# Optimization experiments

Hardware: AMD Instinct MI355X
Metric: run time of the kernel (lower is better)

The kernel has to match this reference:

```python
import jax, jax.numpy as jnp
import numpy as np

K = 3          # kernel size
STRIDE = 1
# padding=0, dilation=1, groups=1 (torchvision DeformConv2d defaults for args not passed)


def _offset_conv(x, w_off, b_off):
    # plain VALID conv, NCHW / OIHW
    out = jax.lax.conv_general_dilated(
        x, w_off, window_strides=(STRIDE, STRIDE), padding='VALID',
        dimension_numbers=('NCHW', 'OIHW', 'NCHW'))
    return out + b_off[None, :, None, None]


def _bilinear_sample(xp, ys, xs):
    # xp: [B,H,W,C]; ys/xs: [B,KK,Ho,Wo] fractional sample coords
    B, H, W, _ = xp.shape
    y0f = jnp.floor(ys)
    x0f = jnp.floor(xs)
    wy = ys - y0f
    wx = xs - x0f
    y0 = y0f.astype(jnp.int32)
    x0 = x0f.astype(jnp.int32)
    b = jnp.arange(B)[:, None, None, None]

    def gather(yi, xi):
        valid = (yi >= 0) & (yi < H) & (xi >= 0) & (xi < W)
        yc = jnp.clip(yi, 0, H - 1)
        xc = jnp.clip(xi, 0, W - 1)
        return xp[b, yc, xc] * valid[..., None].astype(xp.dtype)

    v00 = gather(y0, x0)
    v01 = gather(y0, x0 + 1)
    v10 = gather(y0 + 1, x0)
    v11 = gather(y0 + 1, x0 + 1)
    w00 = ((1 - wy) * (1 - wx))[..., None]
    w01 = ((1 - wy) * wx)[..., None]
    w10 = (wy * (1 - wx))[..., None]
    w11 = (wy * wx)[..., None]
    return v00 * w00 + v01 * w01 + v10 * w10 + v11 * w11  # [B,KK,Ho,Wo,C]


def _mdconv_block(x, w_off, b_off, weight, bias):
    B, Cin, H, W = x.shape
    KK = K * K
    off_out = _offset_conv(x, w_off, b_off)            # [B, 3*KK, Ho, Wo]
    Ho, Wo = off_out.shape[2], off_out.shape[3]
    o1 = off_out[:, :KK]
    o2 = off_out[:, KK:2 * KK]
    mask = jax.nn.sigmoid(off_out[:, 2 * KK:])          # [B,KK,Ho,Wo]
    # torchvision offset layout: pairs (y, x) per kernel point, built as cat(o1, o2)
    off = jnp.concatenate([o1, o2], axis=1).reshape(B, KK, 2, Ho, Wo)
    off_y, off_x = off[:, :, 0], off[:, :, 1]

    kh = jnp.arange(KK) // K
    kw = jnp.arange(KK) % K
    base_y = jnp.arange(Ho)[None, :] * STRIDE + kh[:, None]   # [KK,Ho]
    base_x = jnp.arange(Wo)[None, :] * STRIDE + kw[:, None]   # [KK,Wo]
    ys = base_y[None, :, :, None].astype(x.dtype) + off_y     # [B,KK,Ho,Wo]
    xs = base_x[None, :, None, :].astype(x.dtype) + off_x

    xp = jnp.transpose(x, (0, 2, 3, 1))                        # [B,H,W,Cin]
    sampled = _bilinear_sample(xp, ys, xs)                     # [B,KK,Ho,Wo,Cin]
    sampled = sampled * mask[..., None]                        # modulation
    w = weight.reshape(weight.shape[0], weight.shape[1], KK)   # [Cout,Cin,KK]
    out = jnp.einsum('bkhwc,ock->bohw', sampled, w)
    out = out + bias[None, :, None, None]
    return jax.nn.relu(out)  # block's activate_func=relu; norm/pool are None


def setup_inputs() -> dict:
    key = jax.random.key(0)
    k1, k2, k3, k4, k5 = jax.random.split(key, 5)
    B, Cin, Cout, H, W = 4, 64, 64, 128, 128
    x = jax.random.normal(k1, (B, Cin, H, W), dtype=jnp.float32)
    # offset/mask conv params (original zero-inits; use small random to exercise sampling)
    w_off = jax.random.normal(k2, (3 * K * K, Cin, K, K), dtype=jnp.float32) * 0.1 / np.sqrt(Cin * K * K)
    b_off = jax.random.normal(k3, (3 * K * K,), dtype=jnp.float32) * 0.1
    fan_in = Cin * K * K
    weight = jax.random.uniform(k4, (Cout, Cin, K, K), dtype=jnp.float32,
                                minval=-1.0, maxval=1.0) / np.sqrt(fan_in)
    bias = jax.random.uniform(k5, (Cout,), dtype=jnp.float32,
                              minval=-1.0, maxval=1.0) / np.sqrt(fan_in)
    return {'x': x, 'w_off': w_off, 'b_off': b_off, 'weight': weight, 'bias': bias}


def reference(x, w_off, b_off, weight, bias):
    return _mdconv_block(x, w_off, b_off, weight, bias)
```

## Files before the change

### kernel.cpp

```cpp
#include <hip/hip_runtime.h>
#include <hip/hip_bf16.h>
#include <math.h>

namespace {
constexpr int Bn = 4, Cin = 64, Cout = 64, Hh = 128, Ww = 128, Ho = 126, Wo = 126;
constexpr int HW = Hh * Ww;
constexpr int WOB = 63;
constexpr int NBLK = Bn * Ho * 2;
constexpr int ROWU = 68;
constexpr int RSTR = 346;
}

typedef __attribute__((ext_vector_type(8))) short bf16x8;
typedef __attribute__((ext_vector_type(4))) float f32x4;

__device__ __forceinline__ unsigned short f2bf(float f) {
    __hip_bfloat16 h = __float2bfloat16(f);
    return __builtin_bit_cast(unsigned short, h);
}
__device__ __forceinline__ float bf2f(unsigned short u) {
    unsigned int v = (unsigned int)u << 16;
    return __builtin_bit_cast(float, v);
}
__device__ __forceinline__ unsigned int f2bf_pk(float lo, float hi) {
    return (unsigned int)f2bf(lo) | ((unsigned int)f2bf(hi) << 16);
}
__device__ __forceinline__ bf16x8 mk8(unsigned int u0, unsigned int u1,
                                      unsigned int u2, unsigned int u3) {
    union { unsigned int u[4]; bf16x8 v; } x;
    x.u[0] = u0; x.u[1] = u1; x.u[2] = u2; x.u[3] = u3;
    return x.v;
}
__device__ __forceinline__ int swz_block(int orig, int nwg) {
    int q = nwg >> 3, r = nwg & 7;
    int xcd = orig & 7, idx = orig >> 3;
    return (xcd < r ? xcd * (q + 1) : r * (q + 1) + (xcd - r) * q) + idx;
}

__global__ __launch_bounds__(256) void prep_transpose_kernel(
    const float* __restrict__ x, const float* __restrict__ w_off,
    const float* __restrict__ weight, unsigned int* __restrict__ xT16,
    unsigned short* __restrict__ wA_hi, unsigned short* __restrict__ wA_lo,
    unsigned short* __restrict__ wOff_hi, unsigned short* __restrict__ wOff_lo)
{
    int blk = blockIdx.x;
    if (blk < 1024) {
        __shared__ float t[64][65];
        int b    = blk >> 8;
        int hw0  = (blk & 255) * 64;
        int lane = (int)(threadIdx.x & 63);
        int w4   = (int)(threadIdx.x >> 6);

        const float* xb = x + b * (Cin * HW) + hw0;
#pragma unroll
        for (int i = 0; i < 16; ++i) {
            int cin = w4 * 16 + i;
            t[cin][lane] = xb[cin * HW + lane];
        }
        __syncthreads();
        unsigned int* dst = xT16 + ((size_t)b * HW + hw0) * 32;
        int px = (int)(threadIdx.x >> 2);
        int c8 = (int)(threadIdx.x & 3) * 8;
#pragma unroll
        for (int i = 0; i < 8; ++i) {
            int cp = c8 + i;
            dst[px * 32 + cp] = f2bf_pk(t[2 * cp][px], t[2 * cp + 1][px]);
        }
    } else {
        int i = (blk - 1024) * 256 + (int)threadIdx.x;
        if (i < 36864) {
            int j = i % 8;  int t = i / 8;
            int l = t % 64; t /= 64;
            int h = t % 2;  t /= 2;
            int w = t % 4;  int k = t / 4;
            int cout = 16 * w + (l & 15);
            int cin  = 32 * h + 8 * (l >> 4) + j;
            float v = weight[cout * 576 + cin * 9 + k];
            unsigned short hi = f2bf(v);
            wA_hi[i] = hi;
            wA_lo[i] = f2bf(v - bf2f(hi));

            int o = cout;
            float vo = o < 27 ? w_off[o * 576 + cin * 9 + k] : 0.f;
            unsigned short oh = f2bf(vo);
            wOff_hi[i] = oh;
            wOff_lo[i] = f2bf(vo - bf2f(oh));
        }
    }
}

__global__ __launch_bounds__(256, 2) void mdcn_kernel(
    const unsigned int* __restrict__ xT16, const float* __restrict__ b_off,
    const unsigned short* __restrict__ wOff_hi,
    const unsigned short* __restrict__ wOff_lo,
    const unsigned short* __restrict__ wA_hi,
    const unsigned short* __restrict__ wA_lo,
    const float* __restrict__ bias, float* __restrict__ out)
{
    __shared__ unsigned int region[32 * RSTR];
    __shared__ unsigned int lds[2][32 * ROWU];
    __shared__ float Ap[27][64];

    int wg   = swz_block(blockIdx.x, NBLK);
    int wid  = __builtin_amdgcn_readfirstlane((int)(threadIdx.x >> 6));
    int lane = (int)(threadIdx.x & 63);
    int b    = wg / 252;
    int rem  = wg - b * 252;
    int ho   = rem >> 1;
    int c0   = (rem & 1) * WOB;
    int x_lo = c0 - 1;
    int pxs  = min(lane, 62);
    int wo   = c0 + pxs;

    const unsigned int* xTb = xT16 + (size_t)b * HW * 32;

    for (int i = 0; i < 11; ++i) {
        int idx4 = (int)threadIdx.x + 256 * i;
        if (idx4 < 2720) {
            int cp4 = (idx4 & 7) * 4;
            int rc  = idx4 >> 3;
            int row = rc / 68;
            int col = rc - row * 68;
            int y = min(max(ho - 1 + row, 0), Hh - 1);
            int x = min(max(x_lo + col, 0), Ww - 1);
            uint4 q = *reinterpret_cast<const uint4*>(xTb + (y * Ww + x) * 32 + cp4);
            region[(cp4 + 0) * RSTR + rc] = q.x;
            region[(cp4 + 1) * RSTR + rc] = q.y;
            region[(cp4 + 2) * RSTR + rc] = q.z;
            region[(cp4 + 3) * RSTR + rc] = q.w;
        }
    }
    __syncthreads();

    {
        int ct = wid & 1;
        int t0 = (wid >> 1) * 2;
        f32x4 acc0 = {0.f, 0.f, 0.f, 0.f}, acc1 = acc0;
        int g4 = (lane >> 4) * 4;

#pragma unroll
        for (int k = 0; k < 9; ++k) {
            int kh = k / 3, kw = k - 3 * kh;
            int roff = (kh + 1) * 68 + 1 + kw;
            const bf16x8* waH = reinterpret_cast<const bf16x8*>(
                wOff_hi + ((k * 4 + ct) * 2) * 512 + lane * 8);
            const bf16x8* waL = reinterpret_cast<const bf16x8*>(
                wOff_lo + ((k * 4 + ct) * 2) * 512 + lane * 8);
            bf16x8 a0h = waH[0], a1h = waH[64];
            bf16x8 a0l = waL[0], a1l = waL[64];
#pragma unroll
            for (int tt = 0; tt < 2; ++tt) {
                int px = 16 * (t0 + tt) + (lane & 15);
                int ci = roff + px;
                bf16x8 b0 = mk8(region[(g4 + 0) * RSTR + ci], region[(g4 + 1) * RSTR + ci],
                                region[(g4 + 2) * RSTR + ci], region[(g4 + 3) * RSTR + ci]);
                bf16x8 b1 = mk8(region[(16 + g4 + 0) * RSTR + ci], region[(16 + g4 + 1) * RSTR + ci],
                                region[(16 + g4 + 2) * RSTR + ci], region[(16 + g4 + 3) * RSTR + ci]);
                f32x4& a = tt ? acc1 : acc0;
                a = __builtin_amdgcn_mfma_f32_16x16x32_bf16(a0h, b0, a, 0, 0, 0);
                a = __builtin_amdgcn_mfma_f32_16x16x32_bf16(a0l, b0, a, 0, 0, 0);
                a = __builtin_amdgcn_mfma_f32_16x16x32_bf16(a1h, b1, a, 0, 0, 0);
                a = __builtin_amdgcn_mfma_f32_16x16x32_bf16(a1l, b1, a, 0, 0, 0);
            }
        }

#pragma unroll
        for (int tt = 0; tt < 2; ++tt) {
            f32x4 a = tt ? acc1 : acc0;
            int px = 16 * (t0 + tt) + (lane & 15);
#pragma unroll
            for (int rg = 0; rg < 4; ++rg) {
                int o = 16 * ct + 4 * (lane >> 4) + rg;
                if (o < 27) Ap[o][px] = a[rg];
            }
        }
        __syncthreads();
    }

    auto SAMPLE = [&](int k, int buf) {
        float oy = Ap[2 * k][lane];
        float ox = Ap[2 * k + 1][lane];
        float mv = Ap[18 + k][lane] + b_off[18 + k];
        float ys = (float)(ho + k / 3) + oy + b_off[2 * k];
        float xs = (float)(wo + k % 3) + ox + b_off[2 * k + 1];
        float m  = 1.0f / (1.0f + expf(-mv));
        float y0f = floorf(ys), x0f = floorf(xs);
        float wy = ys - y0f, wx = xs - x0f;
        int y0 = (int)y0f, x0 = (int)x0f;
        float vy0 = (y0 >= 0  && y0 < Hh)     ? 1.f : 0.f;
        float vy1 = (y0 >= -1 && y0 < Hh - 1) ? 1.f : 0.f;
        float vx0 = (x0 >= 0  && x0 < Ww)     ? 1.f : 0.f;
        float vx1 = (x0 >= -1 && x0 < Ww - 1) ? 1.f : 0.f;
        float W00 = (1.f - wy) * (1.f - wx) * m * vy0 * vx0;
        float W01 = (1.f - wy) * wx         * m * vy0 * vx1;
        float W10 = wy         * (1.f - wx) * m * vy1 * vx0;
        float W11 = wy         * wx         * m * vy1 * vx1;

        unsigned int cu00[8], cu01[8], cu10[8], cu11[8];
        bool ok = (y0 >= ho - 1) && (y0 <= ho + 2) &&
                  (x0 >= x_lo) && (x0 <= x_lo + 66);
        if (ok) {
            int s00 = (y0 - (ho - 1)) * 68 + (x0 - x_lo);
#pragma unroll
            for (int j = 0; j < 8; ++j) {
                int basej = (wid * 8 + j) * RSTR + s00;
                cu00[j] = region[basej];
                cu01[j] = region[basej + 1];
                cu10[j] = region[basej + 68];
                cu11[j] = region[basej + 69];
            }
        } else {
            int y0c = min(max(y0, 0), Hh - 1), y1c = min(max(y0 + 1, 0), Hh - 1);
            int x0c = min(max(x0, 0), Ww - 1), x1c = min(max(x0 + 1, 0), Ww - 1);
            const unsigned int* bw = xTb + wid * 8;
            uint4 qa, qb;
            qa = *reinterpret_cast<const uint4*>(bw + (y0c * Ww + x0c) * 32);
            qb = *reinterpret_cast<const uint4*>(bw + (y0c * Ww + x0c) * 32 + 4);
            cu00[0]=qa.x; cu00[1]=qa.y; cu00[2]=qa.z; cu00[3]=qa.w;
            cu00[4]=qb.x; cu00[5]=qb.y; cu00[6]=qb.z; cu00[7]=qb.w;
            qa = *reinterpret_cast<const uint4*>(bw + (y0c * Ww + x1c) * 32);
            qb = *reinterpret_cast<const uint4*>(bw + (y0c * Ww + x1c) * 32 + 4);
            cu01[0]=qa.x; cu01[1]=qa.y; cu01[2]=qa.z; cu01[3]=qa.w;
            cu01[4]=qb.x; cu01[5]=qb.y; cu01[6]=qb.z; cu01[7]=qb.w;
            qa = *reinterpret_cast<const uint4*>(bw + (y1c * Ww + x0c) * 32);
            qb = *reinterpret_cast<const uint4*>(bw + (y1c * Ww + x0c) * 32 + 4);
            cu10[0]=qa.x; cu10[1]=qa.y; cu10[2]=qa.z; cu10[3]=qa.w;
            cu10[4]=qb.x; cu10[5]=qb.y; cu10[6]=qb.z; cu10[7]=qb.w;
            qa = *reinterpret_cast<const uint4*>(bw + (y1c * Ww + x1c) * 32);
            qb = *reinterpret_cast<const uint4*>(bw + (y1c * Ww + x1c) * 32 + 4);
            cu11[0]=qa.x; cu11[1]=qa.y; cu11[2]=qa.z; cu11[3]=qa.w;
            cu11[4]=qb.x; cu11[5]=qb.y; cu11[6]=qb.z; cu11[7]=qb.w;
        }

        unsigned int* dst = &lds[buf][(8 * wid) * ROWU + lane];
#pragma unroll
        for (int j = 0; j < 8; ++j) {
            float c00a = bf2f((unsigned short)(cu00[j] & 0xffff));
            float c00b = bf2f((unsigned short)(cu00[j] >> 16));
            float c01a = bf2f((unsigned short)(cu01[j] & 0xffff));
            float c01b = bf2f((unsigned short)(cu01[j] >> 16));
            float c10a = bf2f((unsigned short)(cu10[j] & 0xffff));
            float c10b = bf2f((unsigned short)(cu10[j] >> 16));
            float c11a = bf2f((unsigned short)(cu11[j] & 0xffff));
            float c11b = bf2f((unsigned short)(cu11[j] >> 16));
            float s0 = W00 * c00a + W01 * c01a;
            s0 = fmaf(W10, c10a, s0); s0 = fmaf(W11, c11a, s0);
            float s1 = W00 * c00b + W01 * c01b;
            s1 = fmaf(W10, c10b, s1); s1 = fmaf(W11, c11b, s1);
            dst[j * ROWU] = f2bf_pk(s0, s1);
        }
    };

    f32x4 acc[4];
#pragma unroll
    for (int t = 0; t < 4; ++t) acc[t] = {0.f, 0.f, 0.f, 0.f};

    SAMPLE(0, 0);
    __syncthreads();

#pragma unroll
    for (int k = 0; k < 9; ++k) {
        int cur = k & 1;
        if (k < 8) SAMPLE(k + 1, cur ^ 1);
        {
            const bf16x8* waH = reinterpret_cast<const bf16x8*>(
                wA_hi + ((k * 4 + wid) * 2) * 512 + lane * 8);
            const bf16x8* waL = reinterpret_cast<const bf16x8*>(
                wA_lo + ((k * 4 + wid) * 2) * 512 + lane * 8);
            bf16x8 a0h = waH[0], a1h = waH[64];
            bf16x8 a0l = waL[0], a1l = waL[64];
            const unsigned int* Lh = &lds[cur][0];
            int g4 = (lane >> 4) * 4;
#pragma unroll
            for (int t = 0; t < 4; ++t) {
                int colp = 16 * t + (lane & 15);
                bf16x8 b0 = mk8(Lh[(g4 + 0) * ROWU + colp], Lh[(g4 + 1) * ROWU + colp],
                                Lh[(g4 + 2) * ROWU + colp], Lh[(g4 + 3) * ROWU + colp]);
                bf16x8 b1 = mk8(Lh[(16 + g4 + 0) * ROWU + colp], Lh[(16 + g4 + 1) * ROWU + colp],
                                Lh[(16 + g4 + 2) * ROWU + colp], Lh[(16 + g4 + 3) * ROWU + colp]);
                acc[t] = __builtin_amdgcn_mfma_f32_16x16x32_bf16(a0h, b0, acc[t], 0, 0, 0);
                acc[t] = __builtin_amdgcn_mfma_f32_16x16x32_bf16(a0l, b0, acc[t], 0, 0, 0);
                acc[t] = __builtin_amdgcn_mfma_f32_16x16x32_bf16(a1h, b1, acc[t], 0, 0, 0);
                acc[t] = __builtin_amdgcn_mfma_f32_16x16x32_bf16(a1l, b1, acc[t], 0, 0, 0);
            }
        }
        __syncthreads();
    }

#pragma unroll
    for (int t = 0; t < 4; ++t) {
        int ps = 16 * t + (lane & 15);
        if (ps >= WOB) continue;
        int col = c0 + ps;
#pragma unroll
        for (int rg = 0; rg < 4; ++rg) {
            int cout = 16 * wid + 4 * (lane >> 4) + rg;
            float v = acc[t][rg] + bias[cout];
            out[((b * Cout + cout) * Ho + ho) * Wo + col] = fmaxf(v, 0.f);
        }
    }
}

extern "C" void kernel_launch(void* const* d_in, const int* in_sizes, int n_in,
                              void* d_out, int out_size, void* d_ws, size_t ws_size,
                              hipStream_t stream)
{
    const float* x      = (const float*)d_in[0];
    const float* w_off  = (const float*)d_in[1];
    const float* b_off  = (const float*)d_in[2];
    const float* weight = (const float*)d_in[3];
    const float* bias   = (const float*)d_in[4];

    unsigned int* xT16 = (unsigned int*)d_ws;
    unsigned short* wA_hi   = (unsigned short*)(xT16 + (size_t)Bn * HW * 32);
    unsigned short* wA_lo   = wA_hi + 36864;
    unsigned short* wOff_hi = wA_lo + 36864;
    unsigned short* wOff_lo = wOff_hi + 36864;

    prep_transpose_kernel<<<1024 + 144, 256, 0, stream>>>(
        x, w_off, weight, xT16, wA_hi, wA_lo, wOff_hi, wOff_lo);
    mdcn_kernel<<<NBLK, 256, 0, stream>>>(xT16, b_off, wOff_hi, wOff_lo,
                                          wA_hi, wA_lo, bias, (float*)d_out);
}
```

Measured before the change: 53.01 us.

## Feed sampled values straight into MFMA registers, dropping LDS staging buffer

Work is re-partitioned so each wave handles 16 output pixels across all 64 output channels instead of 16 output channels across all pixels. Each lane's bilinear samples already match the MFMA B-operand layout, so they go straight into registers. This removes the double-buffered LDS tile and the per-tap __syncthreads. Launch bounds are raised to 3 blocks per SM because LDS use drops. In exchange, each wave now loads all weight fragments for every tap instead of one quarter of them.

```diff
diff --git a/kernel.cpp b/kernel.cpp
--- a/kernel.cpp
+++ b/kernel.cpp
@@ -7,7 +7,6 @@
 constexpr int HW = Hh * Ww;
 constexpr int WOB = 63;
 constexpr int NBLK = Bn * Ho * 2;
-constexpr int ROWU = 68;
 constexpr int RSTR = 346;
 }
 
@@ -89,7 +88,7 @@
     }
 }
 
-__global__ __launch_bounds__(256, 2) void mdcn_kernel(
+__global__ __launch_bounds__(256, 3) void mdcn_kernel(
     const unsigned int* __restrict__ xT16, const float* __restrict__ b_off,
     const unsigned short* __restrict__ wOff_hi,
     const unsigned short* __restrict__ wOff_lo,
@@ -98,7 +97,6 @@
     const float* __restrict__ bias, float* __restrict__ out)
 {
     __shared__ unsigned int region[32 * RSTR];
-    __shared__ unsigned int lds[2][32 * ROWU];
     __shared__ float Ap[27][64];
 
     int wg   = swz_block(blockIdx.x, NBLK);
@@ -109,8 +107,6 @@
     int ho   = rem >> 1;
     int c0   = (rem & 1) * WOB;
     int x_lo = c0 - 1;
-    int pxs  = min(lane, 62);
-    int wo   = c0 + pxs;
 
     const unsigned int* xTb = xT16 + (size_t)b * HW * 32;
 
@@ -177,12 +173,23 @@
         __syncthreads();
     }
 
-    auto SAMPLE = [&](int k, int buf) {
-        float oy = Ap[2 * k][lane];
-        float ox = Ap[2 * k + 1][lane];
-        float mv = Ap[18 + k][lane] + b_off[18 + k];
+    int g  = lane >> 4;
+    int g4 = g * 4;
+    int pl = 16 * wid + (lane & 15);
+    int pls = min(pl, 62);
+    int wol = c0 + pls;
+
+    f32x4 acc[4];
+#pragma unroll
+    for (int ct = 0; ct < 4; ++ct) acc[ct] = {0.f, 0.f, 0.f, 0.f};
+
+#pragma unroll
+    for (int k = 0; k < 9; ++k) {
+        float oy = Ap[2 * k][pl];
+        float ox = Ap[2 * k + 1][pl];
+        float mv = Ap[18 + k][pl] + b_off[18 + k];
         float ys = (float)(ho + k / 3) + oy + b_off[2 * k];
-        float xs = (float)(wo + k % 3) + ox + b_off[2 * k + 1];
+        float xs = (float)(wol + k % 3) + ox + b_off[2 * k + 1];
         float m  = 1.0f / (1.0f + expf(-mv));
         float y0f = floorf(ys), x0f = floorf(xs);
         float wy = ys - y0f, wx = xs - x0f;
@@ -202,37 +209,44 @@
         if (ok) {
             int s00 = (y0 - (ho - 1)) * 68 + (x0 - x_lo);
 #pragma unroll
-            for (int j = 0; j < 8; ++j) {
-                int basej = (wid * 8 + j) * RSTR + s00;
+            for (int j = 0; j < 4; ++j) {
+                int basej = (g4 + j) * RSTR + s00;
                 cu00[j] = region[basej];
                 cu01[j] = region[basej + 1];
                 cu10[j] = region[basej + 68];
                 cu11[j] = region[basej + 69];
             }
+#pragma unroll
+            for (int j = 0; j < 4; ++j) {
+                int basej = (16 + g4 + j) * RSTR + s00;
+                cu00[4 + j] = region[basej];
+                cu01[4 + j] = region[basej + 1];
+                cu10[4 + j] = region[basej + 68];
+                cu11[4 + j] = region[basej + 69];
+            }
         } else {
             int y0c = min(max(y0, 0), Hh - 1), y1c = min(max(y0 + 1, 0), Hh - 1);
             int x0c = min(max(x0, 0), Ww - 1), x1c = min(max(x0 + 1, 0), Ww - 1);
-            const unsigned int* bw = xTb + wid * 8;
             uint4 qa, qb;
-            qa = *reinterpret_cast<const uint4*>(bw + (y0c * Ww + x0c) * 32);
-            qb = *reinterpret_cast<const uint4*>(bw + (y0c * Ww + x0c) * 32 + 4);
+            qa = *reinterpret_cast<const uint4*>(xTb + (y0c * Ww + x0c) * 32 + g4);
+            qb = *reinterpret_cast<const uint4*>(xTb + (y0c * Ww + x0c) * 32 + 16 + g4);
             cu00[0]=qa.x; cu00[1]=qa.y; cu00[2]=qa.z; cu00[3]=qa.w;
             cu00[4]=qb.x; cu00[5]=qb.y; cu00[6]=qb.z; cu00[7]=qb.w;
-            qa = *reinterpret_cast<const uint4*>(bw + (y0c * Ww + x1c) * 32);
-            qb = *reinterpret_cast<const uint4*>(bw + (y0c * Ww + x1c) * 32 + 4);
+            qa = *reinterpret_cast<const uint4*>(xTb + (y0c * Ww + x1c) * 32 + g4);
+            qb = *reinterpret_cast<const uint4*>(xTb + (y0c * Ww + x1c) * 32 + 16 + g4);
             cu01[0]=qa.x; cu01[1]=qa.y; cu01[2]=qa.z; cu01[3]=qa.w;
             cu01[4]=qb.x; cu01[5]=qb.y; cu01[6]=qb.z; cu01[7]=qb.w;
-            qa = *reinterpret_cast<const uint4*>(bw + (y1c * Ww + x0c) * 32);
-            qb = *reinterpret_cast<const uint4*>(bw + (y1c * Ww + x0c) * 32 + 4);
+            qa = *reinterpret_cast<const uint4*>(xTb + (y1c * Ww + x0c) * 32 + g4);
+            qb = *reinterpret_cast<const uint4*>(xTb + (y1c * Ww + x0c) * 32 + 16 + g4);
             cu10[0]=qa.x; cu10[1]=qa.y; cu10[2]=qa.z; cu10[3]=qa.w;
             cu10[4]=qb.x; cu10[5]=qb.y; cu10[6]=qb.z; cu10[7]=qb.w;
-            qa = *reinterpret_cast<const uint4*>(bw + (y1c * Ww + x1c) * 32);
-            qb = *reinterpret_cast<const uint4*>(bw + (y1c * Ww + x1c) * 32 + 4);
+            qa = *reinterpret_cast<const uint4*>(xTb + (y1c * Ww + x1c) * 32 + g4);
+            qb = *reinterpret_cast<const uint4*>(xTb + (y1c * Ww + x1c) * 32 + 16 + g4);
             cu11[0]=qa.x; cu11[1]=qa.y; cu11[2]=qa.z; cu11[3]=qa.w;
             cu11[4]=qb.x; cu11[5]=qb.y; cu11[6]=qb.z; cu11[7]=qb.w;
         }
 
-        unsigned int* dst = &lds[buf][(8 * wid) * ROWU + lane];
+        unsigned int pb[8];
 #pragma unroll
         for (int j = 0; j < 8; ++j) {
             float c00a = bf2f((unsigned short)(cu00[j] & 0xffff));
@@ -247,56 +261,37 @@
             s0 = fmaf(W10, c10a, s0); s0 = fmaf(W11, c11a, s0);
             float s1 = W00 * c00b + W01 * c01b;
             s1 = fmaf(W10, c10b, s1); s1 = fmaf(W11, c11b, s1);
-            dst[j * ROWU] = f2bf_pk(s0, s1);
-        }
-    };
-
-    f32x4 acc[4];
-#pragma unroll
-    for (int t = 0; t < 4; ++t) acc[t] = {0.f, 0.f, 0.f, 0.f};
-
-    SAMPLE(0, 0);
-    __syncthreads();
-
-#pragma unroll
-    for (int k = 0; k < 9; ++k) {
-        int cur = k & 1;
-        if (k < 8) SAMPLE(k + 1, cur ^ 1);
-        {
+            pb[j] = f2bf_pk(s0, s1);
+        }
+        bf16x8 b0 = mk8(pb[0], pb[1], pb[2], pb[3]);
+        bf16x8 b1 = mk8(pb[4], pb[5], pb[6], pb[7]);
+
+#pragma unroll
+        for (int ct = 0; ct < 4; ++ct) {
             const bf16x8* waH = reinterpret_cast<const bf16x8*>(
-                wA_hi + ((k * 4 + wid) * 2) * 512 + lane * 8);
+                wA_hi + ((k * 4 + ct) * 2) * 512 + lane * 8);
             const bf16x8* waL = reinterpret_cast<const bf16x8*>(
-                wA_lo + ((k * 4 + wid) * 2) * 512 + lane * 8);
+                wA_lo + ((k * 4 + ct) * 2) * 512 + lane * 8);
             bf16x8 a0h = waH[0], a1h = waH[64];
             bf16x8 a0l = waL[0], a1l = waL[64];
-            const unsigned int* Lh = &lds[cur][0];
-            int g4 = (lane >> 4) * 4;
-#pragma unroll
-            for (int t = 0; t < 4; ++t) {
-                int colp = 16 * t + (lane & 15);
-                bf16x8 b0 = mk8(Lh[(g4 + 0) * ROWU + colp], Lh[(g4 + 1) * ROWU + colp],
-                                Lh[(g4 + 2) * ROWU + colp], Lh[(g4 + 3) * ROWU + colp]);
-                bf16x8 b1 = mk8(Lh[(16 + g4 + 0) * ROWU + colp], Lh[(16 + g4 + 1) * ROWU + colp],
-                                Lh[(16 + g4 + 2) * ROWU + colp], Lh[(16 + g4 + 3) * ROWU + colp]);
-                acc[t] = __builtin_amdgcn_mfma_f32_16x16x32_bf16(a0h, b0, acc[t], 0, 0, 0);
-                acc[t] = __builtin_amdgcn_mfma_f32_16x16x32_bf16(a0l, b0, acc[t], 0, 0, 0);
-                acc[t] = __builtin_amdgcn_mfma_f32_16x16x32_bf16(a1h, b1, acc[t], 0, 0, 0);
-                acc[t] = __builtin_amdgcn_mfma_f32_16x16x32_bf16(a1l, b1, acc[t], 0, 0, 0);
-            }
-        }
-        __syncthreads();
-    }
-
-#pragma unroll
-    for (int t = 0; t < 4; ++t) {
-        int ps = 16 * t + (lane & 15);
-        if (ps >= WOB) continue;
+            acc[ct] = __builtin_amdgcn_mfma_f32_16x16x32_bf16(a0h, b0, acc[ct], 0, 0, 0);
+            acc[ct] = __builtin_amdgcn_mfma_f32_16x16x32_bf16(a0l, b0, acc[ct], 0, 0, 0);
+            acc[ct] = __builtin_amdgcn_mfma_f32_16x16x32_bf16(a1h, b1, acc[ct], 0, 0, 0);
+            acc[ct] = __builtin_amdgcn_mfma_f32_16x16x32_bf16(a1l, b1, acc[ct], 0, 0, 0);
+        }
+    }
+
+    int ps = 16 * wid + (lane & 15);
+    if (ps < WOB) {
         int col = c0 + ps;
 #pragma unroll
-        for (int rg = 0; rg < 4; ++rg) {
-            int cout = 16 * wid + 4 * (lane >> 4) + rg;
-            float v = acc[t][rg] + bias[cout];
-            out[((b * Cout + cout) * Ho + ho) * Wo + col] = fmaxf(v, 0.f);
+        for (int ct = 0; ct < 4; ++ct) {
+#pragma unroll
+            for (int rg = 0; rg < 4; ++rg) {
+                int cout = 16 * ct + 4 * (lane >> 4) + rg;
+                float v = acc[ct][rg] + bias[cout];
+                out[((b * Cout + cout) * Ho + ho) * Wo + col] = fmaxf(v, 0.f);
+            }
         }
     }
 }
```

Result: slower. 57.78 us (+9.0%).
